# Performance work log

Hardware: AMD Instinct MI355X
Metric: run time of the kernel (lower is better)

The kernel has to match this reference:

```python
import jax, jax.numpy as jnp
import numpy as np

BQ = 64  # query block size
BK = 64  # key block size
PV_SCALE = 1e-3  # pvthreshd (~0..50) -> prob threshold, mirrors int8 P-quantization cutoff


def setup_inputs() -> dict:
    key = jax.random.key(0)
    ks = jax.random.split(key, 6)
    B, H, L, D = 2, 16, 2048, 64
    q = jax.random.normal(ks[0], (B, H, L, D), jnp.float32)
    k = jax.random.normal(ks[1], (B, H, L, D), jnp.float32)
    v = jax.random.normal(ks[2], (B, H, L, D), jnp.float32)
    # per-head tuned thresholds (init defaults / autotune ranges)
    cdfthreshd = 0.85 + 0.14 * jax.random.uniform(ks[3], (H,), jnp.float32)
    simthreshd1 = jax.random.uniform(ks[4], (H,), jnp.float32, minval=-0.3, maxval=0.5)
    pvthreshd = jax.random.uniform(ks[5], (H,), jnp.float32, minval=15.0, maxval=25.0)
    return dict(q=q, k=k, v=v, cdfthreshd=cdfthreshd,
                simthreshd1=simthreshd1, pvthreshd=pvthreshd)


def _sparse_meansim_attention(q, k, v, cdfthreshd, simthreshd1, pvthreshd):
    B, H, L, D = q.shape
    nqb, nkb = L // BQ, L // BK
    scale = 1.0 / jnp.sqrt(jnp.float32(D))

    # smooth_k: subtract per-(B,H) key mean along sequence
    k = k - k.mean(axis=2, keepdims=True)

    qb = q.reshape(B, H, nqb, BQ, D)
    kb = k.reshape(B, H, nkb, BK, D)
    qm = qb.mean(axis=3)  # [B,H,nqb,D]
    km = kb.mean(axis=3)  # [B,H,nkb,D]

    # mean cosine similarity of queries to their block mean -> pooled (prunable) blocks
    qn = jnp.linalg.norm(qb, axis=-1)            # [B,H,nqb,BQ]
    qmn = jnp.linalg.norm(qm, axis=-1)           # [B,H,nqb]
    cos = jnp.einsum('bhnqd,bhnd->bhnq', qb, qm) / (qn * qmn[..., None] + 1e-6)
    pooled = cos.mean(axis=-1) > simthreshd1[None, :, None]  # [B,H,nqb]

    # block-level score map from pooled means, CDF-based top-mass block selection
    s = jnp.einsum('bhid,bhjd->bhij', qm, km) * scale        # [B,H,nqb,nkb]
    p = jax.nn.softmax(s, axis=-1)
    order = jnp.argsort(-p, axis=-1)
    p_sorted = jnp.take_along_axis(p, order, axis=-1)
    excl_cdf = jnp.cumsum(p_sorted, axis=-1) - p_sorted      # exclusive CDF
    keep_sorted = excl_cdf < cdfthreshd[None, :, None, None]
    keep = jnp.take_along_axis(keep_sorted, jnp.argsort(order, axis=-1), axis=-1)

    sink = (jnp.arange(nkb) == 0)  # attention_sink: always keep first key block
    block_mask = keep | (~pooled)[..., None] | sink          # [B,H,nqb,nkb]

    # full attention restricted to selected blocks
    S = jnp.einsum('bhqd,bhkd->bhqk', q, k) * scale          # [B,H,L,L]
    m = jnp.repeat(jnp.repeat(block_mask, BQ, axis=2), BK, axis=3)
    P = jax.nn.softmax(jnp.where(m, S, -jnp.inf), axis=-1)

    # second-stage PV pruning: skip PV accumulation for negligible prob blocks
    Pb = P.reshape(B, H, nqb, BQ, nkb, BK)
    pv_keep = Pb.max(axis=(3, 5)) >= pvthreshd[None, :, None, None] * PV_SCALE
    pv_keep = pv_keep | sink
    Pb = Pb * pv_keep[:, :, :, None, :, None].astype(P.dtype)

    o = jnp.einsum('bhqk,bhkd->bhqd', Pb.reshape(B, H, L, L), v)
    return o


def reference(q, k, v, cdfthreshd, simthreshd1, pvthreshd):
    return _sparse_meansim_attention(q, k, v, cdfthreshd, simthreshd1, pvthreshd)
```

## Files before the change

kernel.cpp:

```cpp
#include <hip/hip_runtime.h>
#include <hip/hip_bf16.h>
#include <math.h>
#include <stdint.h>

#define B 2
#define H 16
#define L 2048
#define D 64
#define NB 32
#define PTS 72

typedef unsigned short u16;
typedef unsigned int u32;
typedef __attribute__((ext_vector_type(2))) unsigned int u32x2;
typedef __attribute__((ext_vector_type(8))) short s16x8;
typedef __attribute__((ext_vector_type(4))) float f32x4;

union FragU { s16x8 v; u32 u[4]; };

__device__ __forceinline__ u32 pkbf(float a, float b) {
  __hip_bfloat162 h = __float22bfloat162_rn(make_float2(a, b));
  union { __hip_bfloat162 h; u32 u; } cv; cv.h = h; return cv.u;
}
__device__ __forceinline__ float bf2f(u32 u16bits) {
  union { u32 u; float f; } c; c.u = u16bits << 16; return c.f;
}
__device__ __forceinline__ void split4(float4 p, u32x2& hi, u32x2& lo) {
  u32 h01 = pkbf(p.x, p.y), h23 = pkbf(p.z, p.w);
  float rx = p.x - bf2f(h01 & 0xffffu);
  float ry = p.y - bf2f(h01 >> 16);
  float rz = p.z - bf2f(h23 & 0xffffu);
  float rw = p.w - bf2f(h23 >> 16);
  hi = (u32x2){h01, h23};
  lo = (u32x2){pkbf(rx, ry), pkbf(rz, rw)};
}

__global__ __launch_bounds__(256) void k_prep(const float* __restrict__ k,
                                              const float* __restrict__ v,
                                              float* __restrict__ ksum,
                                              u16* __restrict__ khi_g,
                                              u16* __restrict__ klo_g,
                                              u16* __restrict__ vthi_g,
                                              u16* __restrict__ vtlo_g,
                                              float* __restrict__ kbmax) {
  int blk = blockIdx.x, bh = blk >> 5, j = blk & 31, t = threadIdx.x;
  __shared__ float vt[64 * 65];
  __shared__ float pk_[4][64];
  __shared__ unsigned bmaxS;
  if (t == 0) bmaxS = 0u;
  size_t base = (size_t)blk * 4096;
  {
    int d = t & 63, g = t >> 6;
    float sk = 0.f;
    for (int r = g * 16; r < g * 16 + 16; ++r) sk += k[base + r * 64 + d];
    pk_[g][d] = sk;
  }
  __syncthreads();
  if (t < 64) ksum[(size_t)blk * 64 + t] = pk_[0][t] + pk_[1][t] + pk_[2][t] + pk_[3][t];

  float rmax = 0.f;
  for (int it = 0; it < 4; ++it) {
    int idx = t + 256 * it, r = idx >> 4, c4 = (idx & 15) * 4;
    float4 f = *(const float4*)(k + base + r * 64 + c4);
    u32x2 hi, lo; split4(f, hi, lo);
    *(u32x2*)(khi_g + base + r * 64 + c4) = hi;
    *(u32x2*)(klo_g + base + r * 64 + c4) = lo;
    float ssq = f.x*f.x + f.y*f.y + f.z*f.z + f.w*f.w;
    ssq += __shfl_xor(ssq, 1); ssq += __shfl_xor(ssq, 2);
    ssq += __shfl_xor(ssq, 4); ssq += __shfl_xor(ssq, 8);
    if ((t & 15) == 0) rmax = fmaxf(rmax, ssq);
    float4 g2 = *(const float4*)(v + base + r * 64 + c4);
    vt[(c4 + 0) * 65 + r] = g2.x;
    vt[(c4 + 1) * 65 + r] = g2.y;
    vt[(c4 + 2) * 65 + r] = g2.z;
    vt[(c4 + 3) * 65 + r] = g2.w;
  }
  if ((t & 15) == 0) atomicMax(&bmaxS, __float_as_uint(rmax));
  __syncthreads();
  if (t == 0) kbmax[blk] = __uint_as_float(bmaxS);
  for (int it = 0; it < 2; ++it) {
    int idx = t + 256 * it, d = idx >> 3, s8 = (idx & 7) * 8;
    const float* vr = &vt[d * 65 + s8];
    float4 f0 = {vr[0], vr[1], vr[2], vr[3]};
    float4 f1 = {vr[4], vr[5], vr[6], vr[7]};
    u32x2 h0, l0, h1, l1;
    split4(f0, h0, l0); split4(f1, h1, l1);
    size_t o = (size_t)bh * 131072 + (size_t)d * 2048 + j * 64 + s8;
    *(u32x2*)(vthi_g + o) = h0; *(u32x2*)(vthi_g + o + 4) = h1;
    *(u32x2*)(vtlo_g + o) = l0; *(u32x2*)(vtlo_g + o + 4) = l1;
  }
}

#define RBM_OFF 36864
#define MS_OFF 53760
#define LINV_OFF 54272
#define LPART_OFF 54784
#define QM_OFF 56832
#define FLG_OFF 57344

__global__ __launch_bounds__(256, 2) void k_attn(
    const float* __restrict__ q,
    const float* __restrict__ ksum,
    const u16* __restrict__ khi_g, const u16* __restrict__ klo_g,
    const u16* __restrict__ vthi_g, const u16* __restrict__ vtlo_g,
    const float* __restrict__ cdfthreshd, const float* __restrict__ simthreshd1,
    const float* __restrict__ pvthreshd, const float* __restrict__ kbmax,
    float* __restrict__ out) {
  int blk = blockIdx.x, bh = blk >> 4, ip = blk & 15, h = bh & (H - 1);
  int t = threadIdx.x, lane = t & 63, w = t >> 6;
  int m16 = lane & 15, quad = lane >> 4;

  __shared__ __align__(16) uint8_t smem[57376];
  u16*   pbase = (u16*)smem;
  u32*   rbm0  = (u32*)(smem + RBM_OFF);
  float* MS    = (float*)(smem + MS_OFF);
  float* linvS = (float*)(smem + LINV_OFF);
  float* lpart = (float*)(smem + LPART_OFF);
  float* qmS   = (float*)(smem + QM_OFF);
  int*   flg   = (int*)(smem + FLG_OFF);
#define PHQ(qb) (pbase + (qb) * 9216)
#define PLQ(qb) (pbase + 4608 + (qb) * 9216)

  const float* qg0 = q + ((size_t)bh * L + (size_t)(2 * ip) * 64) * D;
  const float* qg1 = qg0 + 64 * D;
  const u16* kh = khi_g + (size_t)bh * (L * D);
  const u16* kl = klo_g + (size_t)bh * (L * D);
  const u16* vh = vthi_g + (size_t)bh * (L * D);
  const u16* vl = vtlo_g + (size_t)bh * (L * D);

  s16x8 qhf[2][4][2], qlf[2][4][2];
#pragma unroll
  for (int qb = 0; qb < 2; ++qb) {
    const float* qgq = qb ? qg1 : qg0;
#pragma unroll
    for (int nt = 0; nt < 4; ++nt)
#pragma unroll
      for (int ks = 0; ks < 2; ++ks) {
        const float* p0 = qgq + (16 * nt + m16) * 64 + ks * 32 + quad * 8;
        float4 a = *(const float4*)p0;
        float4 b2 = *(const float4*)(p0 + 4);
        u32x2 ha, la, hb, lb;
        split4(a, ha, la); split4(b2, hb, lb);
        FragU fh, fl;
        fh.u[0] = ha[0]; fh.u[1] = ha[1]; fh.u[2] = hb[0]; fh.u[3] = hb[1];
        fl.u[0] = la[0]; fl.u[1] = la[1]; fl.u[2] = lb[0]; fl.u[3] = lb[1];
        qhf[qb][nt][ks] = fh.v; qlf[qb][nt][ks] = fl.v;
      }
  }
  for (int e = t; e < 2 * 64 * 33; e += 256)
    rbm0[e] = 0x7F800000u;

  if (w == 0 || w == 2) {
    int qb = w >> 1;
    const float* qgq = qb ? qg1 : qg0;
    float s = 0.f;
    for (int r = 0; r < 64; ++r) s += qgq[r * 64 + lane];
    qmS[qb * 64 + lane] = s * (1.f / 64.f);
  }
  if (w == 1) {
    float m = (lane < 32) ? kbmax[bh * 32 + lane] : 0.f;
    for (int off = 16; off; off >>= 1) m = fmaxf(m, __shfl_xor(m, off, 32));
    if (lane == 0) ((float*)flg)[6] = m;
  }
  __syncthreads();

  bool keepj = false;
  if ((w == 0 || w == 2) && lane < 32) {
    int qb = w >> 1, j = lane;
    const float* qmv = qmS + qb * 64;
    const float* ksp = ksum + (size_t)bh * NB * 64 + j * 64;
    float sv = 0.f;
    for (int d = 0; d < 64; ++d) sv += qmv[d] * ksp[d];
    sv *= (1.f / 64.f) * 0.125f;
    float mx = sv;
    for (int off = 16; off; off >>= 1) mx = fmaxf(mx, __shfl_xor(mx, off, 32));
    float p = expf(sv - mx);
    float sum = p;
    for (int off = 16; off; off >>= 1) sum += __shfl_xor(sum, off, 32);
    p /= sum;
    float excl = 0.f;
    for (int u = 0; u < 32; ++u) {
      float pu = __shfl(p, u, 32);
      if ((pu > p) || (pu == p && u < j)) excl += pu;
    }
    keepj = excl < cdfthreshd[h];
  }
  if (w == 1 || w == 3) {
    int qb = w >> 1, r = lane;
    const float* qgq = qb ? qg1 : qg0;
    const float* qmv = qmS + qb * 64;
    float kmax2 = ((float*)flg)[6];
    float dot = 0.f, qn2 = 0.f, qmn2 = 0.f;
    for (int d = 0; d < 64; ++d) {
      float a = qgq[r * 64 + d], b2 = qmv[d];
      dot += a * b2; qn2 += a * a; qmn2 += b2 * b2;
    }
    float cs = dot / (sqrtf(qn2) * sqrtf(qmn2) + 1e-6f);
    float su = cs;
    for (int off = 32; off; off >>= 1) su += __shfl_xor(su, off);
    if (lane == 0) flg[qb] = (su * (1.f / 64.f)) > simthreshd1[h];
    MS[qb * 64 + r] = sqrtf(qn2 * kmax2) * 0.125f;
  }
  __syncthreads();
  if ((w == 0 || w == 2) && lane < 32) {
    int qb = w >> 1;
    bool bit = keepj || !flg[qb] || (lane == 0);
    unsigned long long bal = __ballot(bit);
    if (lane == 0) flg[2 + qb] = (int)(u32)bal;
  }
  __syncthreads();
  u32 mw0 = (u32)flg[2], mw1 = (u32)flg[3];

  float Mq[2][4];
#pragma unroll
  for (int qb = 0; qb < 2; ++qb)
#pragma unroll
    for (int nt = 0; nt < 4; ++nt) Mq[qb][nt] = MS[qb * 64 + 16 * nt + m16];

  float lp[2][4] = {{0.f,0.f,0.f,0.f},{0.f,0.f,0.f,0.f}};
  {
    u32 mwU = mw0 | mw1;
    int j = (int)__builtin_ctz(mwU);
    u32 rm_ = mwU & (mwU - 1);
    s16x8 ka[2][2], kan[2][2];
    {
      const u16* kr0 = kh + (size_t)(j * 64 + 16 * w + m16) * 64 + quad * 8;
      const u16* kl0 = kl + (size_t)(j * 64 + 16 * w + m16) * 64 + quad * 8;
#pragma unroll
      for (int ks = 0; ks < 2; ++ks) {
        ka[ks][0] = *(const s16x8*)(kr0 + ks * 32);
        ka[ks][1] = *(const s16x8*)(kl0 + ks * 32);
      }
    }
    for (;;) {
      int nj = -1;
      if (rm_) {
        nj = (int)__builtin_ctz(rm_); rm_ &= rm_ - 1;
        const u16* nr = kh + (size_t)(nj * 64 + 16 * w + m16) * 64 + quad * 8;
        const u16* nl = kl + (size_t)(nj * 64 + 16 * w + m16) * 64 + quad * 8;
#pragma unroll
        for (int ks = 0; ks < 2; ++ks) {
          kan[ks][0] = *(const s16x8*)(nr + ks * 32);
          kan[ks][1] = *(const s16x8*)(nl + ks * 32);
        }
      }
#pragma unroll
      for (int qb = 0; qb < 2; ++qb) {
        u32 mm = qb ? mw1 : mw0;
        if (!((mm >> j) & 1u)) continue;
        f32x4 acc[4];
#pragma unroll
        for (int nt = 0; nt < 4; ++nt) acc[nt] = (f32x4){0.f, 0.f, 0.f, 0.f};
#pragma unroll
        for (int ks = 0; ks < 2; ++ks)
#pragma unroll
          for (int nt = 0; nt < 4; ++nt) {
            acc[nt] = __builtin_amdgcn_mfma_f32_16x16x32_bf16(ka[ks][0], qhf[qb][nt][ks], acc[nt], 0, 0, 0);
            acc[nt] = __builtin_amdgcn_mfma_f32_16x16x32_bf16(ka[ks][1], qhf[qb][nt][ks], acc[nt], 0, 0, 0);
            acc[nt] = __builtin_amdgcn_mfma_f32_16x16x32_bf16(ka[ks][0], qlf[qb][nt][ks], acc[nt], 0, 0, 0);
          }
#pragma unroll
        for (int nt = 0; nt < 4; ++nt) {
          float vmax = -1e30f;
#pragma unroll
          for (int reg = 0; reg < 4; ++reg) {
            float s = acc[nt][reg] * 0.125f - Mq[qb][nt];
            lp[qb][nt] += __expf(s);
            vmax = fmaxf(vmax, s);
          }
          vmax = fmaxf(vmax, __shfl_xor(vmax, 16));
          vmax = fmaxf(vmax, __shfl_xor(vmax, 32));
          if (quad == 0)
            atomicMin(rbm0 + qb * (64 * 33) + (16 * nt + m16) * 33 + j,
                      __float_as_uint(fmaxf(-vmax, 0.f)));
        }
      }
      if (nj < 0) break;
#pragma unroll
      for (int ks = 0; ks < 2; ++ks) { ka[ks][0] = kan[ks][0]; ka[ks][1] = kan[ks][1]; }
      j = nj;
    }
  }
#pragma unroll
  for (int qb = 0; qb < 2; ++qb)
#pragma unroll
    for (int nt = 0; nt < 4; ++nt) {
      float s = lp[qb][nt];
      s += __shfl_xor(s, 16); s += __shfl_xor(s, 32);
      if (quad == 0) lpart[w * 128 + qb * 64 + 16 * nt + m16] = s;
    }
  __syncthreads();
  if (t < 128) linvS[t] = 1.f / (lpart[t] + lpart[128 + t] + lpart[256 + t] + lpart[384 + t]);
  __syncthreads();

  if (w < 2 && lane < 32) {
    u32 mm = w ? mw1 : mw0;
    bool keep = (mm >> lane) & 1u;
    if (keep && lane != 0) {
      float thr = pvthreshd[h] * 1e-3f;
      const float* lin = linvS + w * 64;
      const u32* rb = rbm0 + w * (64 * 33);
      float mp = 0.f;
      for (int r = 0; r < 64; ++r) {
        float key = __uint_as_float(rb[r * 33 + lane]);
        mp = fmaxf(mp, __expf(-key) * lin[r]);
      }
      keep = mp >= thr;
    }
    unsigned long long bal = __ballot(keep);
    if (lane == 0) flg[4 + w] = (int)(u32)bal;
  }
  __syncthreads();
  u32 gm0 = (u32)flg[4], gm1 = (u32)flg[5];

  float linq[2][4];
#pragma unroll
  for (int qb = 0; qb < 2; ++qb)
#pragma unroll
    for (int nt = 0; nt < 4; ++nt) linq[qb][nt] = linvS[qb * 64 + 16 * nt + m16];
  f32x4 oacc[2][4];
#pragma unroll
  for (int qb = 0; qb < 2; ++qb)
#pragma unroll
    for (int nt = 0; nt < 4; ++nt) oacc[qb][nt] = (f32x4){0.f, 0.f, 0.f, 0.f};

  {
    u32 gmU = gm0 | gm1;
    int j = -1;
    u32 g2 = gmU;
    s16x8 ka[2][2];
    if (g2) {
      j = (int)__builtin_ctz(g2); g2 &= g2 - 1;
      const u16* kr0 = kh + (size_t)(j * 64 + 16 * w + m16) * 64 + quad * 8;
      const u16* kl0 = kl + (size_t)(j * 64 + 16 * w + m16) * 64 + quad * 8;
#pragma unroll
      for (int ks = 0; ks < 2; ++ks) {
        ka[ks][0] = *(const s16x8*)(kr0 + ks * 32);
        ka[ks][1] = *(const s16x8*)(kl0 + ks * 32);
      }
    }
    while (j >= 0) {
      int in0 = (gm0 >> j) & 1, in1 = (gm1 >> j) & 1;
      s16x8 va[2][2];
      {
        const u16* vr0 = vh + (size_t)(16 * w + m16) * L + j * 64 + quad * 8;
        const u16* vl0 = vl + (size_t)(16 * w + m16) * L + j * 64 + quad * 8;
#pragma unroll
        for (int ks = 0; ks < 2; ++ks) {
          va[ks][0] = *(const s16x8*)(vr0 + ks * 32);
          va[ks][1] = *(const s16x8*)(vl0 + ks * 32);
        }
      }
      f32x4 acc[4];
      if (in0) {
#pragma unroll
        for (int nt = 0; nt < 4; ++nt) acc[nt] = (f32x4){0.f, 0.f, 0.f, 0.f};
#pragma unroll
        for (int ks = 0; ks < 2; ++ks)
#pragma unroll
          for (int nt = 0; nt < 4; ++nt) {
            acc[nt] = __builtin_amdgcn_mfma_f32_16x16x32_bf16(ka[ks][0], qhf[0][nt][ks], acc[nt], 0, 0, 0);
            acc[nt] = __builtin_amdgcn_mfma_f32_16x16x32_bf16(ka[ks][1], qhf[0][nt][ks], acc[nt], 0, 0, 0);
            acc[nt] = __builtin_amdgcn_mfma_f32_16x16x32_bf16(ka[ks][0], qlf[0][nt][ks], acc[nt], 0, 0, 0);
          }
      }
      __syncthreads();
      if (in0) {
#pragma unroll
        for (int nt = 0; nt < 4; ++nt) {
          float4 pv;
          pv.x = __expf(acc[nt][0] * 0.125f - Mq[0][nt]) * linq[0][nt];
          pv.y = __expf(acc[nt][1] * 0.125f - Mq[0][nt]) * linq[0][nt];
          pv.z = __expf(acc[nt][2] * 0.125f - Mq[0][nt]) * linq[0][nt];
          pv.w = __expf(acc[nt][3] * 0.125f - Mq[0][nt]) * linq[0][nt];
          u32x2 hi, lo; split4(pv, hi, lo);
          int off = (16 * nt + m16) * PTS + 16 * w + 4 * quad;
          *(u32x2*)(PHQ(0) + off) = hi;
          *(u32x2*)(PLQ(0) + off) = lo;
        }
      }
      if (in1) {
#pragma unroll
        for (int nt = 0; nt < 4; ++nt) acc[nt] = (f32x4){0.f, 0.f, 0.f, 0.f};
#pragma unroll
        for (int ks = 0; ks < 2; ++ks)
#pragma unroll
          for (int nt = 0; nt < 4; ++nt) {
            acc[nt] = __builtin_amdgcn_mfma_f32_16x16x32_bf16(ka[ks][0], qhf[1][nt][ks], acc[nt], 0, 0, 0);
            acc[nt] = __builtin_amdgcn_mfma_f32_16x16x32_bf16(ka[ks][1], qhf[1][nt][ks], acc[nt], 0, 0, 0);
            acc[nt] = __builtin_amdgcn_mfma_f32_16x16x32_bf16(ka[ks][0], qlf[1][nt][ks], acc[nt], 0, 0, 0);
          }
#pragma unroll
        for (int nt = 0; nt < 4; ++nt) {
          float4 pv;
          pv.x = __expf(acc[nt][0] * 0.125f - Mq[1][nt]) * linq[1][nt];
          pv.y = __expf(acc[nt][1] * 0.125f - Mq[1][nt]) * linq[1][nt];
          pv.z = __expf(acc[nt][2] * 0.125f - Mq[1][nt]) * linq[1][nt];
          pv.w = __expf(acc[nt][3] * 0.125f - Mq[1][nt]) * linq[1][nt];
          u32x2 hi, lo; split4(pv, hi, lo);
          int off = (16 * nt + m16) * PTS + 16 * w + 4 * quad;
          *(u32x2*)(PHQ(1) + off) = hi;
          *(u32x2*)(PLQ(1) + off) = lo;
        }
      }
      int nj = -1;
      if (g2) {
        nj = (int)__builtin_ctz(g2); g2 &= g2 - 1;
        const u16* nr = kh + (size_t)(nj * 64 + 16 * w + m16) * 64 + quad * 8;
        const u16* nl = kl + (size_t)(nj * 64 + 16 * w + m16) * 64 + quad * 8;
#pragma unroll
        for (int ks = 0; ks < 2; ++ks) {
          ka[ks][0] = *(const s16x8*)(nr + ks * 32);
          ka[ks][1] = *(const s16x8*)(nl + ks * 32);
        }
      }
      __syncthreads();
#pragma unroll
      for (int qb = 0; qb < 2; ++qb) {
        if (!(qb ? in1 : in0)) continue;
        const u16* ph_ = PHQ(qb);
        const u16* pl_ = PLQ(qb);
#pragma unroll
        for (int ks = 0; ks < 2; ++ks)
#pragma unroll
          for (int nt = 0; nt < 4; ++nt) {
            s16x8 pbh = *(const s16x8*)(ph_ + (16 * nt + m16) * PTS + ks * 32 + quad * 8);
            s16x8 pbl = *(const s16x8*)(pl_ + (16 * nt + m16) * PTS + ks * 32 + quad * 8);
            oacc[qb][nt] = __builtin_amdgcn_mfma_f32_16x16x32_bf16(va[ks][0], pbh, oacc[qb][nt], 0, 0, 0);
            oacc[qb][nt] = __builtin_amdgcn_mfma_f32_16x16x32_bf16(va[ks][1], pbh, oacc[qb][nt], 0, 0, 0);
            oacc[qb][nt] = __builtin_amdgcn_mfma_f32_16x16x32_bf16(va[ks][0], pbl, oacc[qb][nt], 0, 0, 0);
          }
      }
      j = nj;
    }
  }

#pragma unroll
  for (int qb = 0; qb < 2; ++qb) {
    float* ob = out + ((size_t)bh * L + (size_t)(2 * ip + qb) * 64) * D;
#pragma unroll
    for (int nt = 0; nt < 4; ++nt)
      *(f32x4*)(ob + (16 * nt + m16) * 64 + 16 * w + 4 * quad) = oacc[qb][nt];
  }
}

extern "C" void kernel_launch(void* const* d_in, const int* in_sizes, int n_in,
                              void* d_out, int out_size, void* d_ws, size_t ws_size,
                              hipStream_t stream) {
  (void)in_sizes; (void)n_in; (void)out_size; (void)ws_size;
  const float* q   = (const float*)d_in[0];
  const float* k   = (const float*)d_in[1];
  const float* v   = (const float*)d_in[2];
  const float* cdf = (const float*)d_in[3];
  const float* sim = (const float*)d_in[4];
  const float* pvt = (const float*)d_in[5];
  float* out = (float*)d_out;

  uint8_t* w8 = (uint8_t*)d_ws;
  float* ksum  = (float*)w8;
  float* kbmax = (float*)(w8 + 262144);
  u16* khi_g  = (u16*)(w8 + 266240);
  u16* klo_g  = khi_g + (size_t)B * H * L * D;
  u16* vthi_g = klo_g + (size_t)B * H * L * D;
  u16* vtlo_g = vthi_g + (size_t)B * H * L * D;

  k_prep<<<B * H * NB, 256, 0, stream>>>(k, v, ksum, khi_g, klo_g, vthi_g, vtlo_g, kbmax);
  k_attn<<<B * H * NB / 2, 256, 0, stream>>>(q, ksum, khi_g, klo_g, vthi_g, vtlo_g,
                                             cdf, sim, pvt, kbmax, out);
}
```

Measured before the change: 224.5 us.

## Deepen K/V register prefetch, stage Q through LDS, use nontemporal loads/stores

The first attention pass now prefetches K fragments two blocks ahead instead of one. The PV pass prefetches both the next K and V fragments at the top of the loop, where before V was loaded on demand and K was fetched late. Q is staged once into padded shared memory with nontemporal loads, so the later mean and cosine passes read LDS rather than global memory. k_prep fuses the key column sum into its main load loop, and the output stores and input loads use nontemporal hints. The deeper prefetching raises register pressure, which could lower occupancy or cause spills under the existing launch bounds.

```diff
diff --git a/kernel.cpp b/kernel.cpp
--- a/kernel.cpp
+++ b/kernel.cpp
@@ -25,14 +25,20 @@
 __device__ __forceinline__ float bf2f(u32 u16bits) {
   union { u32 u; float f; } c; c.u = u16bits << 16; return c.f;
 }
-__device__ __forceinline__ void split4(float4 p, u32x2& hi, u32x2& lo) {
-  u32 h01 = pkbf(p.x, p.y), h23 = pkbf(p.z, p.w);
-  float rx = p.x - bf2f(h01 & 0xffffu);
-  float ry = p.y - bf2f(h01 >> 16);
-  float rz = p.z - bf2f(h23 & 0xffffu);
-  float rw = p.w - bf2f(h23 >> 16);
+__device__ __forceinline__ void split4(f32x4 p, u32x2& hi, u32x2& lo) {
+  u32 h01 = pkbf(p[0], p[1]), h23 = pkbf(p[2], p[3]);
+  float rx = p[0] - bf2f(h01 & 0xffffu);
+  float ry = p[1] - bf2f(h01 >> 16);
+  float rz = p[2] - bf2f(h23 & 0xffffu);
+  float rw = p[3] - bf2f(h23 >> 16);
   hi = (u32x2){h01, h23};
   lo = (u32x2){pkbf(rx, ry), pkbf(rz, rw)};
+}
+__device__ __forceinline__ f32x4 ntld4(const float* p) {
+  return __builtin_nontemporal_load((const f32x4*)p);
+}
+__device__ __forceinline__ void ntst4(float* p, f32x4 v) {
+  __builtin_nontemporal_store(v, (f32x4*)p);
 }
 
 __global__ __launch_bounds__(256) void k_prep(const float* __restrict__ k,
@@ -45,44 +51,46 @@
                                               float* __restrict__ kbmax) {
   int blk = blockIdx.x, bh = blk >> 5, j = blk & 31, t = threadIdx.x;
   __shared__ float vt[64 * 65];
-  __shared__ float pk_[4][64];
+  __shared__ float pk_[16][64];
   __shared__ unsigned bmaxS;
   if (t == 0) bmaxS = 0u;
   size_t base = (size_t)blk * 4096;
-  {
-    int d = t & 63, g = t >> 6;
-    float sk = 0.f;
-    for (int r = g * 16; r < g * 16 + 16; ++r) sk += k[base + r * 64 + d];
-    pk_[g][d] = sk;
-  }
-  __syncthreads();
-  if (t < 64) ksum[(size_t)blk * 64 + t] = pk_[0][t] + pk_[1][t] + pk_[2][t] + pk_[3][t];
-
+  int c4 = (t & 15) * 4, rg = t >> 4;
+  float cs0 = 0.f, cs1 = 0.f, cs2 = 0.f, cs3 = 0.f;
   float rmax = 0.f;
+#pragma unroll
   for (int it = 0; it < 4; ++it) {
-    int idx = t + 256 * it, r = idx >> 4, c4 = (idx & 15) * 4;
-    float4 f = *(const float4*)(k + base + r * 64 + c4);
+    int r = rg + 16 * it;
+    f32x4 f = ntld4(k + base + r * 64 + c4);
+    cs0 += f[0]; cs1 += f[1]; cs2 += f[2]; cs3 += f[3];
     u32x2 hi, lo; split4(f, hi, lo);
     *(u32x2*)(khi_g + base + r * 64 + c4) = hi;
     *(u32x2*)(klo_g + base + r * 64 + c4) = lo;
-    float ssq = f.x*f.x + f.y*f.y + f.z*f.z + f.w*f.w;
+    float ssq = f[0]*f[0] + f[1]*f[1] + f[2]*f[2] + f[3]*f[3];
     ssq += __shfl_xor(ssq, 1); ssq += __shfl_xor(ssq, 2);
     ssq += __shfl_xor(ssq, 4); ssq += __shfl_xor(ssq, 8);
     if ((t & 15) == 0) rmax = fmaxf(rmax, ssq);
-    float4 g2 = *(const float4*)(v + base + r * 64 + c4);
-    vt[(c4 + 0) * 65 + r] = g2.x;
-    vt[(c4 + 1) * 65 + r] = g2.y;
-    vt[(c4 + 2) * 65 + r] = g2.z;
-    vt[(c4 + 3) * 65 + r] = g2.w;
-  }
+    f32x4 g2 = ntld4(v + base + r * 64 + c4);
+    vt[(c4 + 0) * 65 + r] = g2[0];
+    vt[(c4 + 1) * 65 + r] = g2[1];
+    vt[(c4 + 2) * 65 + r] = g2[2];
+    vt[(c4 + 3) * 65 + r] = g2[3];
+  }
+  pk_[rg][c4] = cs0; pk_[rg][c4 + 1] = cs1; pk_[rg][c4 + 2] = cs2; pk_[rg][c4 + 3] = cs3;
   if ((t & 15) == 0) atomicMax(&bmaxS, __float_as_uint(rmax));
   __syncthreads();
+  if (t < 64) {
+    float s = 0.f;
+#pragma unroll
+    for (int g = 0; g < 16; ++g) s += pk_[g][t];
+    ksum[(size_t)blk * 64 + t] = s;
+  }
   if (t == 0) kbmax[blk] = __uint_as_float(bmaxS);
   for (int it = 0; it < 2; ++it) {
     int idx = t + 256 * it, d = idx >> 3, s8 = (idx & 7) * 8;
     const float* vr = &vt[d * 65 + s8];
-    float4 f0 = {vr[0], vr[1], vr[2], vr[3]};
-    float4 f1 = {vr[4], vr[5], vr[6], vr[7]};
+    f32x4 f0 = {vr[0], vr[1], vr[2], vr[3]};
+    f32x4 f1 = {vr[4], vr[5], vr[6], vr[7]};
     u32x2 h0, l0, h1, l1;
     split4(f0, h0, l0); split4(f1, h1, l1);
     size_t o = (size_t)bh * 131072 + (size_t)d * 2048 + j * 64 + s8;
@@ -112,6 +120,7 @@
 
   __shared__ __align__(16) uint8_t smem[57376];
   u16*   pbase = (u16*)smem;
+  float* qfp   = (float*)smem;
   u32*   rbm0  = (u32*)(smem + RBM_OFF);
   float* MS    = (float*)(smem + MS_OFF);
   float* linvS = (float*)(smem + LINV_OFF);
@@ -122,23 +131,31 @@
 #define PLQ(qb) (pbase + 4608 + (qb) * 9216)
 
   const float* qg0 = q + ((size_t)bh * L + (size_t)(2 * ip) * 64) * D;
-  const float* qg1 = qg0 + 64 * D;
   const u16* kh = khi_g + (size_t)bh * (L * D);
   const u16* kl = klo_g + (size_t)bh * (L * D);
   const u16* vh = vthi_g + (size_t)bh * (L * D);
   const u16* vl = vtlo_g + (size_t)bh * (L * D);
 
+  for (int it = 0; it < 8; ++it) {
+    int idx = t + 256 * it;
+    int qb = idx >> 10, rem = idx & 1023;
+    int r = rem >> 4, c4 = (rem & 15) * 4;
+    f32x4 f = ntld4(qg0 + qb * 4096 + r * 64 + c4);
+    *(f32x4*)&qfp[qb * 4352 + r * 68 + c4] = f;
+  }
+  for (int e = t; e < 2 * 64 * 33; e += 256) rbm0[e] = 0x7F800000u;
+  __syncthreads();
+
   s16x8 qhf[2][4][2], qlf[2][4][2];
 #pragma unroll
-  for (int qb = 0; qb < 2; ++qb) {
-    const float* qgq = qb ? qg1 : qg0;
+  for (int qb = 0; qb < 2; ++qb)
 #pragma unroll
     for (int nt = 0; nt < 4; ++nt)
 #pragma unroll
       for (int ks = 0; ks < 2; ++ks) {
-        const float* p0 = qgq + (16 * nt + m16) * 64 + ks * 32 + quad * 8;
-        float4 a = *(const float4*)p0;
-        float4 b2 = *(const float4*)(p0 + 4);
+        const float* p0 = qfp + qb * 4352 + (16 * nt + m16) * 68 + ks * 32 + quad * 8;
+        f32x4 a = *(const f32x4*)p0;
+        f32x4 b2 = *(const f32x4*)(p0 + 4);
         u32x2 ha, la, hb, lb;
         split4(a, ha, la); split4(b2, hb, lb);
         FragU fh, fl;
@@ -146,15 +163,11 @@
         fl.u[0] = la[0]; fl.u[1] = la[1]; fl.u[2] = lb[0]; fl.u[3] = lb[1];
         qhf[qb][nt][ks] = fh.v; qlf[qb][nt][ks] = fl.v;
       }
-  }
-  for (int e = t; e < 2 * 64 * 33; e += 256)
-    rbm0[e] = 0x7F800000u;
 
   if (w == 0 || w == 2) {
     int qb = w >> 1;
-    const float* qgq = qb ? qg1 : qg0;
     float s = 0.f;
-    for (int r = 0; r < 64; ++r) s += qgq[r * 64 + lane];
+    for (int r = 0; r < 64; ++r) s += qfp[qb * 4352 + r * 68 + lane];
     qmS[qb * 64 + lane] = s * (1.f / 64.f);
   }
   if (w == 1) {
@@ -187,12 +200,11 @@
   }
   if (w == 1 || w == 3) {
     int qb = w >> 1, r = lane;
-    const float* qgq = qb ? qg1 : qg0;
     const float* qmv = qmS + qb * 64;
     float kmax2 = ((float*)flg)[6];
     float dot = 0.f, qn2 = 0.f, qmn2 = 0.f;
     for (int d = 0; d < 64; ++d) {
-      float a = qgq[r * 64 + d], b2 = qmv[d];
+      float a = qfp[qb * 4352 + r * 68 + d], b2 = qmv[d];
       dot += a * b2; qn2 += a * a; qmn2 += b2 * b2;
     }
     float cs = dot / (sqrtf(qn2) * sqrtf(qmn2) + 1e-6f);
@@ -220,34 +232,45 @@
   float lp[2][4] = {{0.f,0.f,0.f,0.f},{0.f,0.f,0.f,0.f}};
   {
     u32 mwU = mw0 | mw1;
-    int j = (int)__builtin_ctz(mwU);
-    u32 rm_ = mwU & (mwU - 1);
-    s16x8 ka[2][2], kan[2][2];
+    u32 rm_ = mwU;
+    int j0 = (int)__builtin_ctz(rm_); rm_ &= rm_ - 1;
+    s16x8 ka[2][2], kb_[2][2], kc[2][2];
     {
-      const u16* kr0 = kh + (size_t)(j * 64 + 16 * w + m16) * 64 + quad * 8;
-      const u16* kl0 = kl + (size_t)(j * 64 + 16 * w + m16) * 64 + quad * 8;
+      const u16* kr0 = kh + (size_t)(j0 * 64 + 16 * w + m16) * 64 + quad * 8;
+      const u16* kl0 = kl + (size_t)(j0 * 64 + 16 * w + m16) * 64 + quad * 8;
 #pragma unroll
       for (int ks = 0; ks < 2; ++ks) {
         ka[ks][0] = *(const s16x8*)(kr0 + ks * 32);
         ka[ks][1] = *(const s16x8*)(kl0 + ks * 32);
       }
     }
+    int j1 = -1;
+    if (rm_) {
+      j1 = (int)__builtin_ctz(rm_); rm_ &= rm_ - 1;
+      const u16* nr = kh + (size_t)(j1 * 64 + 16 * w + m16) * 64 + quad * 8;
+      const u16* nl = kl + (size_t)(j1 * 64 + 16 * w + m16) * 64 + quad * 8;
+#pragma unroll
+      for (int ks = 0; ks < 2; ++ks) {
+        kb_[ks][0] = *(const s16x8*)(nr + ks * 32);
+        kb_[ks][1] = *(const s16x8*)(nl + ks * 32);
+      }
+    }
     for (;;) {
-      int nj = -1;
+      int j2 = -1;
       if (rm_) {
-        nj = (int)__builtin_ctz(rm_); rm_ &= rm_ - 1;
-        const u16* nr = kh + (size_t)(nj * 64 + 16 * w + m16) * 64 + quad * 8;
-        const u16* nl = kl + (size_t)(nj * 64 + 16 * w + m16) * 64 + quad * 8;
+        j2 = (int)__builtin_ctz(rm_); rm_ &= rm_ - 1;
+        const u16* nr = kh + (size_t)(j2 * 64 + 16 * w + m16) * 64 + quad * 8;
+        const u16* nl = kl + (size_t)(j2 * 64 + 16 * w + m16) * 64 + quad * 8;
 #pragma unroll
         for (int ks = 0; ks < 2; ++ks) {
-          kan[ks][0] = *(const s16x8*)(nr + ks * 32);
-          kan[ks][1] = *(const s16x8*)(nl + ks * 32);
+          kc[ks][0] = *(const s16x8*)(nr + ks * 32);
+          kc[ks][1] = *(const s16x8*)(nl + ks * 32);
         }
       }
 #pragma unroll
       for (int qb = 0; qb < 2; ++qb) {
         u32 mm = qb ? mw1 : mw0;
-        if (!((mm >> j) & 1u)) continue;
+        if (!((mm >> j0) & 1u)) continue;
         f32x4 acc[4];
 #pragma unroll
         for (int nt = 0; nt < 4; ++nt) acc[nt] = (f32x4){0.f, 0.f, 0.f, 0.f};
@@ -271,14 +294,17 @@
           vmax = fmaxf(vmax, __shfl_xor(vmax, 16));
           vmax = fmaxf(vmax, __shfl_xor(vmax, 32));
           if (quad == 0)
-            atomicMin(rbm0 + qb * (64 * 33) + (16 * nt + m16) * 33 + j,
+            atomicMin(rbm0 + qb * (64 * 33) + (16 * nt + m16) * 33 + j0,
                       __float_as_uint(fmaxf(-vmax, 0.f)));
         }
       }
-      if (nj < 0) break;
-#pragma unroll
-      for (int ks = 0; ks < 2; ++ks) { ka[ks][0] = kan[ks][0]; ka[ks][1] = kan[ks][1]; }
-      j = nj;
+      if (j1 < 0) break;
+#pragma unroll
+      for (int ks = 0; ks < 2; ++ks) {
+        ka[ks][0] = kb_[ks][0]; ka[ks][1] = kb_[ks][1];
+        kb_[ks][0] = kc[ks][0]; kb_[ks][1] = kc[ks][1];
+      }
+      j0 = j1; j1 = j2;
     }
   }
 #pragma unroll
@@ -325,32 +351,40 @@
     for (int nt = 0; nt < 4; ++nt) oacc[qb][nt] = (f32x4){0.f, 0.f, 0.f, 0.f};
 
   {
-    u32 gmU = gm0 | gm1;
+    u32 g2 = gm0 | gm1;
     int j = -1;
-    u32 g2 = gmU;
-    s16x8 ka[2][2];
+    s16x8 ka[2][2], va[2][2], kan[2][2], van[2][2];
     if (g2) {
       j = (int)__builtin_ctz(g2); g2 &= g2 - 1;
       const u16* kr0 = kh + (size_t)(j * 64 + 16 * w + m16) * 64 + quad * 8;
       const u16* kl0 = kl + (size_t)(j * 64 + 16 * w + m16) * 64 + quad * 8;
+      const u16* vr0 = vh + (size_t)(16 * w + m16) * L + j * 64 + quad * 8;
+      const u16* vl0 = vl + (size_t)(16 * w + m16) * L + j * 64 + quad * 8;
 #pragma unroll
       for (int ks = 0; ks < 2; ++ks) {
         ka[ks][0] = *(const s16x8*)(kr0 + ks * 32);
         ka[ks][1] = *(const s16x8*)(kl0 + ks * 32);
+        va[ks][0] = *(const s16x8*)(vr0 + ks * 32);
+        va[ks][1] = *(const s16x8*)(vl0 + ks * 32);
       }
     }
     while (j >= 0) {
+      int nj = -1;
+      if (g2) {
+        nj = (int)__builtin_ctz(g2); g2 &= g2 - 1;
+        const u16* nr = kh + (size_t)(nj * 64 + 16 * w + m16) * 64 + quad * 8;
+        const u16* nl = kl + (size_t)(nj * 64 + 16 * w + m16) * 64 + quad * 8;
+        const u16* vr0 = vh + (size_t)(16 * w + m16) * L + nj * 64 + quad * 8;
+        const u16* vl0 = vl + (size_t)(16 * w + m16) * L + nj * 64 + quad * 8;
+#pragma unroll
+        for (int ks = 0; ks < 2; ++ks) {
+          kan[ks][0] = *(const s16x8*)(nr + ks * 32);
+          kan[ks][1] = *(const s16x8*)(nl + ks * 32);
+          van[ks][0] = *(const s16x8*)(vr0 + ks * 32);
+          van[ks][1] = *(const s16x8*)(vl0 + ks * 32);
+        }
+      }
       int in0 = (gm0 >> j) & 1, in1 = (gm1 >> j) & 1;
-      s16x8 va[2][2];
-      {
-        const u16* vr0 = vh + (size_t)(16 * w + m16) * L + j * 64 + quad * 8;
-        const u16* vl0 = vl + (size_t)(16 * w + m16) * L + j * 64 + quad * 8;
-#pragma unroll
-        for (int ks = 0; ks < 2; ++ks) {
-          va[ks][0] = *(const s16x8*)(vr0 + ks * 32);
-          va[ks][1] = *(const s16x8*)(vl0 + ks * 32);
-        }
-      }
       f32x4 acc[4];
       if (in0) {
 #pragma unroll
@@ -368,11 +402,11 @@
       if (in0) {
 #pragma unroll
         for (int nt = 0; nt < 4; ++nt) {
-          float4 pv;
-          pv.x = __expf(acc[nt][0] * 0.125f - Mq[0][nt]) * linq[0][nt];
-          pv.y = __expf(acc[nt][1] * 0.125f - Mq[0][nt]) * linq[0][nt];
-          pv.z = __expf(acc[nt][2] * 0.125f - Mq[0][nt]) * linq[0][nt];
-          pv.w = __expf(acc[nt][3] * 0.125f - Mq[0][nt]) * linq[0][nt];
+          f32x4 pv;
+          pv[0] = __expf(acc[nt][0] * 0.125f - Mq[0][nt]) * linq[0][nt];
+          pv[1] = __expf(acc[nt][1] * 0.125f - Mq[0][nt]) * linq[0][nt];
+          pv[2] = __expf(acc[nt][2] * 0.125f - Mq[0][nt]) * linq[0][nt];
+          pv[3] = __expf(acc[nt][3] * 0.125f - Mq[0][nt]) * linq[0][nt];
           u32x2 hi, lo; split4(pv, hi, lo);
           int off = (16 * nt + m16) * PTS + 16 * w + 4 * quad;
           *(u32x2*)(PHQ(0) + off) = hi;
@@ -392,26 +426,15 @@
           }
 #pragma unroll
         for (int nt = 0; nt < 4; ++nt) {
-          float4 pv;
-          pv.x = __expf(acc[nt][0] * 0.125f - Mq[1][nt]) * linq[1][nt];
-          pv.y = __expf(acc[nt][1] * 0.125f - Mq[1][nt]) * linq[1][nt];
-          pv.z = __expf(acc[nt][2] * 0.125f - Mq[1][nt]) * linq[1][nt];
-          pv.w = __expf(acc[nt][3] * 0.125f - Mq[1][nt]) * linq[1][nt];
+          f32x4 pv;
+          pv[0] = __expf(acc[nt][0] * 0.125f - Mq[1][nt]) * linq[1][nt];
+          pv[1] = __expf(acc[nt][1] * 0.125f - Mq[1][nt]) * linq[1][nt];
+          pv[2] = __expf(acc[nt][2] * 0.125f - Mq[1][nt]) * linq[1][nt];
+          pv[3] = __expf(acc[nt][3] * 0.125f - Mq[1][nt]) * linq[1][nt];
           u32x2 hi, lo; split4(pv, hi, lo);
           int off = (16 * nt + m16) * PTS + 16 * w + 4 * quad;
           *(u32x2*)(PHQ(1) + off) = hi;
           *(u32x2*)(PLQ(1) + off) = lo;
-        }
-      }
-      int nj = -1;
-      if (g2) {
-        nj = (int)__builtin_ctz(g2); g2 &= g2 - 1;
-        const u16* nr = kh + (size_t)(nj * 64 + 16 * w + m16) * 64 + quad * 8;
-        const u16* nl = kl + (size_t)(nj * 64 + 16 * w + m16) * 64 + quad * 8;
-#pragma unroll
-        for (int ks = 0; ks < 2; ++ks) {
-          ka[ks][0] = *(const s16x8*)(nr + ks * 32);
-          ka[ks][1] = *(const s16x8*)(nl + ks * 32);
         }
       }
       __syncthreads();
@@ -431,6 +454,11 @@
             oacc[qb][nt] = __builtin_amdgcn_mfma_f32_16x16x32_bf16(va[ks][0], pbl, oacc[qb][nt], 0, 0, 0);
           }
       }
+#pragma unroll
+      for (int ks = 0; ks < 2; ++ks) {
+        ka[ks][0] = kan[ks][0]; ka[ks][1] = kan[ks][1];
+        va[ks][0] = van[ks][0]; va[ks][1] = van[ks][1];
+      }
       j = nj;
     }
   }
@@ -440,7 +468,7 @@
     float* ob = out + ((size_t)bh * L + (size_t)(2 * ip + qb) * 64) * D;
 #pragma unroll
     for (int nt = 0; nt < 4; ++nt)
-      *(f32x4*)(ob + (16 * nt + m16) * 64 + 16 * w + 4 * quad) = oacc[qb][nt];
+      ntst4(ob + (16 * nt + m16) * 64 + 16 * w + 4 * quad, oacc[qb][nt]);
   }
 }
 
```

Result: slower. 277.7 us (+23.7%).
